# Kernel tuning notes

Hardware: AMD Instinct MI355X
Metric: run time of the kernel (lower is better)

The kernel has to match this reference:

```python
import jax, jax.numpy as jnp
import numpy as np

N_HEAD = 16
D_HEAD = 64
N_GROUPS = 4
D_EMBED = 1024
ROPE_N = 32
B, T = 2, 2048


def apply_rope(x, cos, sin):
    # x: (..., T, ROPE_N); cos/sin: (T, ROPE_N) broadcast over leading dims
    h = x.shape[-1]
    x1, x2 = x[..., : h // 2], x[..., h // 2 :]
    rotated = jnp.concatenate((-x2, x1), axis=-1)
    return (x * cos + rotated * sin).astype(x.dtype)


def setup_inputs() -> dict:
    key = jax.random.key(0)
    k1, k2, k3, k4, k5 = jax.random.split(key, 5)
    return {
        "x": jax.random.normal(k1, (B, T, D_EMBED), dtype=jnp.float32),
        "cos": jax.random.uniform(k2, (T, ROPE_N), dtype=jnp.float32),
        "sin": jax.random.uniform(k3, (T, ROPE_N), dtype=jnp.float32),
        "mask": jnp.ones((B, T), dtype=bool),  # unused by the original forward (passes None to SDPA)
        "Wqkv": jax.random.normal(k4, (D_EMBED, (N_HEAD + 2 * N_GROUPS) * D_HEAD), dtype=jnp.float32) * 0.02,
        "Wout": jax.random.normal(k5, (N_HEAD * D_HEAD, D_EMBED), dtype=jnp.float32) * 0.02,
    }


def reference(x, cos, sin, mask, Wqkv, Wout):
    Bv, Tv, _ = x.shape
    q_per_kv = N_HEAD // N_GROUPS  # 4
    total_qkv = q_per_kv + 2       # 6

    qkv = jnp.einsum("btc,cf->btf", x, Wqkv)  # (B, T, 1536)
    qkv = qkv.reshape(Bv, Tv, N_GROUPS, total_qkv, D_HEAD)
    qkv = jnp.transpose(qkv, (0, 2, 3, 1, 4))  # (B, G, total_qkv, T, d)

    q = qkv[:, :, :q_per_kv]           # (B, G, q_per_kv, T, d)
    k = qkv[:, :, q_per_kv : q_per_kv + 1]  # (B, G, 1, T, d)
    v = qkv[:, :, q_per_kv + 1 :]           # (B, G, 1, T, d)

    # GQA expand (1 < groups < heads)
    k = jnp.broadcast_to(k, (Bv, N_GROUPS, q_per_kv, Tv, D_HEAD))
    v = jnp.broadcast_to(v, (Bv, N_GROUPS, q_per_kv, Tv, D_HEAD))

    q = q.reshape(Bv, N_HEAD, Tv, D_HEAD)
    k = k.reshape(Bv, N_HEAD, Tv, D_HEAD)
    v = v.reshape(Bv, N_HEAD, Tv, D_HEAD)

    # partial RoPE on the first ROPE_N dims of each head
    q = jnp.concatenate((apply_rope(q[..., :ROPE_N], cos, sin), q[..., ROPE_N:]), axis=-1)
    k = jnp.concatenate((apply_rope(k[..., :ROPE_N], cos, sin), k[..., ROPE_N:]), axis=-1)

    scale = 1.0 / np.sqrt(D_HEAD).astype(np.float32)
    scores = jnp.einsum("bhtd,bhsd->bhts", q, k) * scale
    attn = jax.nn.softmax(scores, axis=-1)
    y = jnp.einsum("bhts,bhsd->bhtd", attn, v)   # (B, H, T, d)
    y = jnp.transpose(y, (0, 2, 1, 3)).reshape(Bv, Tv, N_HEAD * D_HEAD)
    return jnp.einsum("btf,fc->btc", y, Wout)
```

## Files before the change

### kernel.cpp

```cpp
#include <hip/hip_runtime.h>
#include <hip/hip_bf16.h>
#include <math.h>

#define BATCH   2
#define TSEQ    2048
#define DEMBED  1024
#define NHEAD   16
#define DHEAD   64
#define NGROUP  4
#define ROPEN   32
#define FQKV    1536
#define MROWS   (BATCH*TSEQ)

typedef __attribute__((ext_vector_type(8))) short short8;
typedef __attribute__((ext_vector_type(4))) float floatx4;

__device__ __forceinline__ void split_pack8(const float* f, uint4& h4, uint4& l4) {
    uint u[8], lu[8];
    #pragma unroll
    for (int j = 0; j < 8; ++j) {
        u[j] = __float_as_uint(f[j]);
        float lf = f[j] - __uint_as_float(u[j] & 0xffff0000u);
        lu[j] = __float_as_uint(lf);
    }
    h4.x = __builtin_amdgcn_perm(u[1], u[0], 0x07060302u);
    h4.y = __builtin_amdgcn_perm(u[3], u[2], 0x07060302u);
    h4.z = __builtin_amdgcn_perm(u[5], u[4], 0x07060302u);
    h4.w = __builtin_amdgcn_perm(u[7], u[6], 0x07060302u);
    l4.x = __builtin_amdgcn_perm(lu[1], lu[0], 0x07060302u);
    l4.y = __builtin_amdgcn_perm(lu[3], lu[2], 0x07060302u);
    l4.z = __builtin_amdgcn_perm(lu[5], lu[4], 0x07060302u);
    l4.w = __builtin_amdgcn_perm(lu[7], lu[6], 0x07060302u);
}

__device__ __forceinline__ void rtn_pack8(const float* f, uint4& h4) {
    uint t[8];
    #pragma unroll
    for (int j = 0; j < 8; ++j)
        t[j] = __float_as_uint(f[j]) + 0x8000u;
    h4.x = __builtin_amdgcn_perm(t[1], t[0], 0x07060302u);
    h4.y = __builtin_amdgcn_perm(t[3], t[2], 0x07060302u);
    h4.z = __builtin_amdgcn_perm(t[5], t[4], 0x07060302u);
    h4.w = __builtin_amdgcn_perm(t[7], t[6], 0x07060302u);
}

__device__ __forceinline__ uint pk_bf16x2(float f0, float f1) {
    uint u0 = __float_as_uint(f0) + 0x8000u;
    uint u1 = __float_as_uint(f1) + 0x8000u;
    return __builtin_amdgcn_perm(u1, u0, 0x07060302u);
}

__device__ __forceinline__ float fast_exp2(float x) {
    float r;
    asm("v_exp_f32 %0, %1" : "=v"(r) : "v"(x));
    return r;
}

__device__ __forceinline__ void lds_async16(void* lds, const void* gp) {
    __builtin_amdgcn_global_load_lds(
        (const __attribute__((address_space(1))) unsigned int*)gp,
        (__attribute__((address_space(3))) unsigned int*)lds,
        16, 0, 0);
}


__global__ __launch_bounds__(256) void conv_xy(const float* __restrict__ in,
                                               char* __restrict__ img) {
    const int tid = threadIdx.x;
    const int c   = blockIdx.x & 15;
    const int mt  = blockIdx.x >> 4;
    const int r    = tid >> 1;
    const int half = tid & 1;

    const float* src = in + (size_t)(mt*128 + r)*1024 + c*64 + half*32;
    float f[32];
    #pragma unroll
    for (int u = 0; u < 8; ++u)
        *(float4*)(f + 4*u) = *(const float4*)(src + 4*u);

    char* tile = img + ((size_t)(mt*16 + c)) * 32768;
    #pragma unroll
    for (int cc = 0; cc < 4; ++cc) {
        uint4 h4, l4;
        split_pack8(f + cc*8, h4, l4);
        int j    = half*4 + cc;
        int phys = j ^ (r & 7);
        *(uint4*)(tile + r*128 + phys*16)         = h4;
        *(uint4*)(tile + 16384 + r*128 + phys*16) = l4;
    }
}

__global__ __launch_bounds__(256) void conv_w(const float* __restrict__ W,
                                              int N,
                                              char* __restrict__ img) {
    __shared__ float Lf[64][132];
    const int tid = threadIdx.x;
    const int c   = blockIdx.x;
    const int nt  = blockIdx.y;

    {
        const int kk = tid >> 2;
        const int nc = (tid & 3) * 32;
        const float* src = W + (size_t)(c*64 + kk)*N + nt*128 + nc;
        #pragma unroll
        for (int u = 0; u < 8; ++u)
            *(float4*)(&Lf[kk][nc + 4*u]) = *(const float4*)(src + 4*u);
    }
    __syncthreads();

    char* tile = img + ((size_t)(nt*16 + c)) * 32768;
    #pragma unroll
    for (int rep = 0; rep < 4; ++rep) {
        int idx = rep*256 + tid;
        int n = idx & 127;
        int j = idx >> 7;
        float v[8];
        #pragma unroll
        for (int i = 0; i < 8; ++i) v[i] = Lf[j*8 + i][n];
        uint4 h4, l4;
        split_pack8(v, h4, l4);
        int phys = j ^ (n & 7);
        *(uint4*)(tile + n*128 + phys*16)         = h4;
        *(uint4*)(tile + 16384 + n*128 + phys*16) = l4;
    }
}

struct GemmAcc { floatx4 a[4][4]; };

__device__ __forceinline__ void gemm_mfma_core(const char* __restrict__ Aimg,
                                               const char* __restrict__ Bimg,
                                               char* smem, int mt, int nt,
                                               int tid, GemmAcc& G) {
    const int wv = tid >> 6;
    const int wm = wv & 1, wn = wv >> 1;
    const int lane = tid & 63;
    const int qd = lane >> 4, cl = lane & 15;
    const int wslot = (tid & 192) * 16;

    #pragma unroll
    for (int tm = 0; tm < 4; ++tm)
        #pragma unroll
        for (int tn = 0; tn < 4; ++tn)
            G.a[tm][tn] = (floatx4){0.f, 0.f, 0.f, 0.f};

    for (int c = 0; c < 16; ++c) {
        __syncthreads();
        {
            const uint4* gA = (const uint4*)(Aimg + ((size_t)(mt*16 + c)) * 32768) + tid;
            const uint4* gB = (const uint4*)(Bimg + ((size_t)(nt*16 + c)) * 32768) + tid;
            #pragma unroll
            for (int j = 0; j < 8; ++j) {
                lds_async16(smem + j*4096 + wslot,         gA + j*256);
                lds_async16(smem + 32768 + j*4096 + wslot, gB + j*256);
            }
        }
        __syncthreads();

        #pragma unroll
        for (int s = 0; s < 2; ++s) {
            const int phys = ((s*4 + qd) ^ (cl & 7)) * 16;
            short8 ah[4], al[4], bh[4], bl[4];
            #pragma unroll
            for (int tt = 0; tt < 4; ++tt) {
                const int rA = wm*64 + 16*tt + cl;
                ah[tt] = *(const short8*)(smem + rA*128 + phys);
                al[tt] = *(const short8*)(smem + 16384 + rA*128 + phys);
                const int rB = wn*64 + 16*tt + cl;
                bh[tt] = *(const short8*)(smem + 32768 + rB*128 + phys);
                bl[tt] = *(const short8*)(smem + 49152 + rB*128 + phys);
            }
            #pragma unroll
            for (int tm = 0; tm < 4; ++tm)
                #pragma unroll
                for (int tn = 0; tn < 4; ++tn) {
                    G.a[tm][tn] = __builtin_amdgcn_mfma_f32_16x16x32_bf16(ah[tm], bh[tn], G.a[tm][tn], 0, 0, 0);
                    G.a[tm][tn] = __builtin_amdgcn_mfma_f32_16x16x32_bf16(al[tm], bh[tn], G.a[tm][tn], 0, 0, 0);
                    G.a[tm][tn] = __builtin_amdgcn_mfma_f32_16x16x32_bf16(ah[tm], bl[tn], G.a[tm][tn], 0, 0, 0);
                }
        }
    }
}

__global__ __launch_bounds__(256, 2) void gemm_qkv_mfma(const char* __restrict__ Aimg,
                                                        const char* __restrict__ Bimg,
                                                        const float* __restrict__ cosp,
                                                        const float* __restrict__ sinp,
                                                        float* __restrict__ Qf,
                                                        ushort* __restrict__ Kimg,
                                                        ushort* __restrict__ Vimg) {
    __shared__ __align__(16) char smem[68608];
    const int tid = threadIdx.x;
    const int nt = blockIdx.x, mt = blockIdx.y;

    GemmAcc G;
    gemm_mfma_core(Aimg, Bimg, smem, mt, nt, tid, G);

    const int wv = tid >> 6;
    const int wm = wv & 1, wn = wv >> 1;
    const int lane = tid & 63;
    const int qd = lane >> 4, cl = lane & 15;

    const int slice = nt*2 + wn;
    const int g  = slice / 6;
    const int jj = slice % 6;
    const int b  = mt >> 4;

    if (jj != 5) {
        #pragma unroll
        for (int tm = 0; tm < 4; ++tm)
            #pragma unroll
            for (int r = 0; r < 4; ++r) {
                int m = mt*128 + wm*64 + 16*tm + 4*qd + r;
                int t = m & 2047;
                float c1 = cosp[t*ROPEN + cl],      s1 = sinp[t*ROPEN + cl];
                float c2 = cosp[t*ROPEN + 16 + cl], s2 = sinp[t*ROPEN + 16 + cl];
                float x1 = G.a[tm][0][r], x2 = G.a[tm][1][r];
                G.a[tm][0][r] = x1*c1 - x2*s1;
                G.a[tm][1][r] = x2*c2 + x1*s2;
            }
    }

    if (jj < 4) {
        #pragma unroll
        for (int tm = 0; tm < 4; ++tm)
            #pragma unroll
            for (int tn = 0; tn < 4; ++tn)
                #pragma unroll
                for (int r = 0; r < 4; ++r) {
                    int m = mt*128 + wm*64 + 16*tm + 4*qd + r;
                    Qf[(size_t)m*1024 + (g*4 + jj)*64 + 16*tn + cl] = G.a[tm][tn][r];
                }
    } else {
        float* Lw = (float*)(smem + wv*17152);
        __syncthreads();
        #pragma unroll
        for (int tm = 0; tm < 4; ++tm)
            #pragma unroll
            for (int tn = 0; tn < 4; ++tn)
                #pragma unroll
                for (int r = 0; r < 4; ++r)
                    Lw[(16*tm + 4*qd + r)*67 + 16*tn + cl] = G.a[tm][tn][r];
        __syncthreads();

        const int cloc = (mt & 15)*2 + wm;
        ushort* img = ((jj == 4) ? Kimg : Vimg)
                      + (size_t)(b*4 + g)*262144 + (size_t)cloc*8192;
        if (jj == 4) {
            const int rr = lane;
            float f[8];
            #pragma unroll
            for (int ch = 0; ch < 8; ++ch) {
                *(float4*)f       = *(const float4*)(&Lw[rr*67 + ch*8]);
                *(float4*)(f + 4) = *(const float4*)(&Lw[rr*67 + ch*8 + 4]);
                uint4 h4, l4;
                split_pack8(f, h4, l4);
                int phys = ch ^ (rr & 7);
                *(uint4*)(img + rr*64 + phys*8)        = h4;
                *(uint4*)(img + 4096 + rr*64 + phys*8) = l4;
            }
        } else {
            const int d = lane;
            float f[8];
            #pragma unroll
            for (int ch = 0; ch < 8; ++ch) {
                const int kb = 32*(ch >> 2) + 4*(ch & 3);
                #pragma unroll
                for (int i = 0; i < 4; ++i) f[i]     = Lw[(kb + i)*67 + d];
                #pragma unroll
                for (int i = 0; i < 4; ++i) f[4 + i] = Lw[(kb + 16 + i)*67 + d];
                uint4 h4;
                rtn_pack8(f, h4);
                int phys = ch ^ (d & 7);
                *(uint4*)(img + d*64 + phys*8) = h4;
            }
        }
    }
}

__global__ __launch_bounds__(256, 2) void gemm_out_mfma(const char* __restrict__ Aimg,
                                                        const char* __restrict__ Bimg,
                                                        float* __restrict__ C) {
    __shared__ __align__(16) char smem[49152];
    const int tid = threadIdx.x;
    const int nt = blockIdx.x, mt = blockIdx.y;

    const int wv = tid >> 6;
    const int wm = wv & 1, wn = wv >> 1;
    const int lane = tid & 63;
    const int qd = lane >> 4, cl = lane & 15;
    const int wslot = (tid & 192) * 16;

    floatx4 acc[2][4];
    #pragma unroll
    for (int tm = 0; tm < 2; ++tm)
        #pragma unroll
        for (int tn = 0; tn < 4; ++tn)
            acc[tm][tn] = (floatx4){0.f, 0.f, 0.f, 0.f};

    for (int c = 0; c < 16; ++c) {
        __syncthreads();
        {
            const char* sA = Aimg + ((size_t)((mt >> 1)*16 + c))*32768
                                  + (mt & 1)*8192 + (size_t)tid*16;
            const char* sB = Bimg + ((size_t)(nt*16 + c))*32768 + (size_t)tid*16;
            lds_async16(smem + wslot,          sA);
            lds_async16(smem + 4096  + wslot,  sA + 4096);
            lds_async16(smem + 8192  + wslot,  sA + 16384);
            lds_async16(smem + 12288 + wslot,  sA + 16384 + 4096);
            #pragma unroll
            for (int j = 0; j < 4; ++j) {
                lds_async16(smem + 16384 + j*4096 + wslot, sB + j*4096);
                lds_async16(smem + 32768 + j*4096 + wslot, sB + 16384 + j*4096);
            }
        }
        __syncthreads();

        #pragma unroll
        for (int s = 0; s < 2; ++s) {
            const int phys = ((s*4 + qd) ^ (cl & 7)) * 16;
            short8 ah[2], al[2], bh[4], bl[4];
            #pragma unroll
            for (int tt = 0; tt < 2; ++tt) {
                const int rA = wm*32 + 16*tt + cl;
                ah[tt] = *(const short8*)(smem + rA*128 + phys);
                al[tt] = *(const short8*)(smem + 8192 + rA*128 + phys);
            }
            #pragma unroll
            for (int tt = 0; tt < 4; ++tt) {
                const int rB = wn*64 + 16*tt + cl;
                bh[tt] = *(const short8*)(smem + 16384 + rB*128 + phys);
                bl[tt] = *(const short8*)(smem + 32768 + rB*128 + phys);
            }
            #pragma unroll
            for (int tm = 0; tm < 2; ++tm)
                #pragma unroll
                for (int tn = 0; tn < 4; ++tn) {
                    acc[tm][tn] = __builtin_amdgcn_mfma_f32_16x16x32_bf16(ah[tm], bh[tn], acc[tm][tn], 0, 0, 0);
                    acc[tm][tn] = __builtin_amdgcn_mfma_f32_16x16x32_bf16(al[tm], bh[tn], acc[tm][tn], 0, 0, 0);
                    acc[tm][tn] = __builtin_amdgcn_mfma_f32_16x16x32_bf16(ah[tm], bl[tn], acc[tm][tn], 0, 0, 0);
                }
        }
    }

    #pragma unroll
    for (int tm = 0; tm < 2; ++tm)
        #pragma unroll
        for (int tn = 0; tn < 4; ++tn)
            #pragma unroll
            for (int r = 0; r < 4; ++r) {
                int m = mt*64 + wm*32 + 16*tm + 4*qd + r;
                int n = nt*128 + wn*64 + 16*tn + cl;
                C[(size_t)m*1024 + n] = acc[tm][tn][r];
            }
}

__global__ __launch_bounds__(512, 4) void attn15(const float* __restrict__ Qf,
                                                 const char* __restrict__ Kimg,
                                                 const char* __restrict__ Vimg,
                                                 char* __restrict__ Yimg) {
    __shared__ __align__(16) char smem[49152];

    const int tid  = threadIdx.x;
    const int wv8  = tid >> 6;
    const int grp  = wv8 >> 2;
    const int wq   = wv8 & 3;
    const int lane = tid & 63;
    const int qd   = lane >> 4;
    const int cl   = lane & 15;

    const int bg    = blockIdx.x & 7;
    const int inner = blockIdx.x >> 3;
    const int hj    = inner >> 4;
    const int qt    = inner & 15;
    const int b = bg >> 2, g = bg & 3;
    const int h = g*4 + hj;

    short8 qh[2][2], ql[2][2];
    #pragma unroll
    for (int rb = 0; rb < 2; ++rb) {
        const float* qp = Qf + (size_t)(b*2048 + qt*128 + wq*32 + rb*16 + cl)*1024
                             + h*64 + 8*qd;
        #pragma unroll
        for (int s = 0; s < 2; ++s) {
            float f[8];
            *(float4*)f       = *(const float4*)(qp + 32*s);
            *(float4*)(f + 4) = *(const float4*)(qp + 32*s + 4);
            #pragma unroll
            for (int i = 0; i < 8; ++i) f[i] *= 0.125f * 1.44269504088896f;
            uint4 h4, l4;
            split_pack8(f, h4, l4);
            qh[rb][s] = __builtin_bit_cast(short8, h4);
            ql[rb][s] = __builtin_bit_cast(short8, l4);
        }
    }

    floatx4 accOT[2][4] = {};
    float lsum[2] = {};

    const char* Kg0 = Kimg + (size_t)bg*524288;
    const char* Vg0 = Vimg + (size_t)bg*524288;
    const int wslot = wv8 << 10;

    int voff[4];
    #pragma unroll
    for (int tt = 0; tt < 4; ++tt)
        voff[tt] = (16*tt + cl)*128 + (((4*grp + qd) ^ (cl & 7))*16);

    {
        const char* ksrc = Kg0 + (size_t)tid*16;
        lds_async16(smem + wslot,        ksrc);
        lds_async16(smem + 8192 + wslot, ksrc + 8192);
        lds_async16(smem + 32768 + wslot, Vg0 + (size_t)tid*16);
    }

    for (int c = 0; c < TSEQ/64; ++c) {
        __syncthreads();
        const int buf = c & 1;

        if (c + 1 < TSEQ/64) {
            const char* ksrc = Kg0 + (size_t)(c+1)*16384 + (size_t)tid*16;
            const char* vsrc = Vg0 + (size_t)(c+1)*16384 + (size_t)tid*16;
            lds_async16(smem + (1-buf)*16384 + wslot,        ksrc);
            lds_async16(smem + (1-buf)*16384 + 8192 + wslot, ksrc + 8192);
            lds_async16(smem + 32768 + (1-buf)*8192 + wslot, vsrc);
        }
        const char* Kl = smem + buf*16384;
        const char* Vl = smem + 32768 + buf*8192;

        floatx4 accST[2][2] = {};
        __builtin_amdgcn_s_setprio(1);
        #pragma unroll
        for (int s = 0; s < 2; ++s) {
            #pragma unroll
            for (int tt = 0; tt < 2; ++tt) {
                const int off = (32*grp + 16*tt + cl)*128
                              + (((4*s + qd) ^ (cl & 7))*16);
                short8 kh = *(const short8*)(Kl + off);
                short8 kl = *(const short8*)(Kl + 8192 + off);
                #pragma unroll
                for (int rb = 0; rb < 2; ++rb) {
                    accST[rb][tt] = __builtin_amdgcn_mfma_f32_16x16x32_bf16(kh, qh[rb][s], accST[rb][tt], 0, 0, 0);
                    accST[rb][tt] = __builtin_amdgcn_mfma_f32_16x16x32_bf16(kh, ql[rb][s], accST[rb][tt], 0, 0, 0);
                    accST[rb][tt] = __builtin_amdgcn_mfma_f32_16x16x32_bf16(kl, qh[rb][s], accST[rb][tt], 0, 0, 0);
                }
            }
        }
        __builtin_amdgcn_s_setprio(0);

        short8 pa[2];
        #pragma unroll
        for (int rb = 0; rb < 2; ++rb) {
            float p[8];
            #pragma unroll
            for (int tt = 0; tt < 2; ++tt)
                #pragma unroll
                for (int r = 0; r < 4; ++r)
                    p[4*tt + r] = fast_exp2(accST[rb][tt][r]);
            lsum[rb] += ((p[0] + p[1]) + (p[2] + p[3]))
                      + ((p[4] + p[5]) + (p[6] + p[7]));
            uint4 paw;
            paw.x = pk_bf16x2(p[0], p[1]);
            paw.y = pk_bf16x2(p[2], p[3]);
            paw.z = pk_bf16x2(p[4], p[5]);
            paw.w = pk_bf16x2(p[6], p[7]);
            pa[rb] = __builtin_bit_cast(short8, paw);
        }

        __builtin_amdgcn_s_setprio(1);
        #pragma unroll
        for (int tt = 0; tt < 4; ++tt) {
            short8 vh = *(const short8*)(Vl + voff[tt]);
            #pragma unroll
            for (int rb = 0; rb < 2; ++rb)
                accOT[rb][tt] = __builtin_amdgcn_mfma_f32_16x16x32_bf16(vh, pa[rb], accOT[rb][tt], 0, 0, 0);
        }
        __builtin_amdgcn_s_setprio(0);
    }

    __syncthreads();
    float* Pb = (float*)smem;
    if (grp == 1) {
        #pragma unroll
        for (int rb = 0; rb < 2; ++rb) {
            float* dst = Pb + (size_t)(((wq*2 + rb)*64) + lane)*17;
            #pragma unroll
            for (int tt = 0; tt < 4; ++tt)
                #pragma unroll
                for (int r = 0; r < 4; ++r)
                    dst[4*tt + r] = accOT[rb][tt][r];
            dst[16] = lsum[rb];
        }
    }
    __syncthreads();
    float inv[2] = {1.f, 1.f};
    if (grp == 0) {
        #pragma unroll
        for (int rb = 0; rb < 2; ++rb) {
            const float* sp = Pb + (size_t)(((wq*2 + rb)*64) + lane)*17;
            #pragma unroll
            for (int tt = 0; tt < 4; ++tt)
                #pragma unroll
                for (int r = 0; r < 4; ++r)
                    accOT[rb][tt][r] += sp[4*tt + r];
            float l = lsum[rb] + sp[16];
            l += __shfl_xor(l, 16);
            l += __shfl_xor(l, 32);
            inv[rb] = 1.0f / l;
        }
    }
    __syncthreads();
    float* Lt = (float*)smem;
    if (grp == 0) {
        #pragma unroll
        for (int rb = 0; rb < 2; ++rb) {
            const int row = wq*32 + rb*16 + cl;
            #pragma unroll
            for (int tt = 0; tt < 4; ++tt)
                #pragma unroll
                for (int r = 0; r < 4; ++r)
                    Lt[row*66 + 16*tt + 4*qd + r] = accOT[rb][tt][r] * inv[rb];
        }
    }
    __syncthreads();
    {
        char* tile = Yimg + (size_t)((b*16 + qt)*16 + h) * 32768;
        #pragma unroll
        for (int cc = 0; cc < 2; ++cc) {
            const int idx = tid*2 + cc;
            const int r0 = idx >> 3;
            const int j  = idx & 7;
            float f[8];
            #pragma unroll
            for (int u = 0; u < 4; ++u)
                *(float2*)(f + 2*u) = *(const float2*)(&Lt[r0*66 + j*8 + 2*u]);
            uint4 h4, l4;
            split_pack8(f, h4, l4);
            int phys = j ^ (r0 & 7);
            *(uint4*)(tile + r0*128 + phys*16)         = h4;
            *(uint4*)(tile + 16384 + r0*128 + phys*16) = l4;
        }
    }
}

extern "C" void kernel_launch(void* const* d_in, const int* in_sizes, int n_in,
                              void* d_out, int out_size, void* d_ws, size_t ws_size,
                              hipStream_t stream) {
    const float* x    = (const float*)d_in[0];
    const float* cosp = (const float*)d_in[1];
    const float* sinp = (const float*)d_in[2];
    const float* Wqkv = (const float*)d_in[4];
    const float* Wout = (const float*)d_in[5];
    float* out = (float*)d_out;

    char* ws = (char*)d_ws;
    float*  Qf    = (float*)(ws);
    ushort* Kimg  = (ushort*)(ws + ((size_t)16<<20));
    ushort* Vimg  = (ushort*)(ws + ((size_t)20<<20));
    char*   Bo    = ws + ((size_t)24<<20);
    char*   Ximg  = ws + ((size_t)28<<20);
    char*   Bq    = ws + ((size_t)44<<20);
    char*   Yimg  = ws + ((size_t)28<<20);

    conv_xy<<<512, 256, 0, stream>>>(x, Ximg);
    conv_w<<<dim3(16, 12), 256, 0, stream>>>(Wqkv, FQKV, Bq);
    conv_w<<<dim3(16, 8), 256, 0, stream>>>(Wout, DEMBED, Bo);
    gemm_qkv_mfma<<<dim3(12, 32), 256, 0, stream>>>(Ximg, Bq, cosp, sinp,
                                                    Qf, Kimg, Vimg);
    attn15<<<512, 512, 0, stream>>>(Qf, (const char*)Kimg, (const char*)Vimg,
                                    Yimg);
    gemm_out_mfma<<<dim3(8, 64), 256, 0, stream>>>(Yimg, Bo, out);
}
```

Before: 224.2 us.

## Double-buffer LDS tiles in both GEMM kernels with half-K chunks

Both MFMA GEMM kernels now split each K chunk into two half-chunks and double-buffer them in LDS. The async global-to-LDS copy of the next half-chunk is issued before computing on the current one, and one of the two barriers per iteration is dropped. Global reads use a new per-thread swizzled offset so LDS reads follow a 64-byte-row XOR pattern. The aim is to hide load latency behind MFMA work, at the cost of twice as many loop iterations and more address registers, and the pattern relies on the async copies having completed by the single barrier.

New measurement: 229.0 us. 1.02x slower.

```diff
diff --git a/kernel.cpp b/kernel.cpp
--- a/kernel.cpp
+++ b/kernel.cpp
@@ -136,6 +136,19 @@
     const int lane = tid & 63;
     const int qd = lane >> 4, cl = lane & 15;
     const int wslot = (tid & 192) * 16;
+    const int xorv  = (cl >> 1) & 3;
+
+    int soff[2][2];
+    #pragma unroll
+    for (int jj = 0; jj < 2; ++jj) {
+        const int ci   = jj*256 + tid;
+        const int row  = ci >> 2;
+        const int slot = ci & 3;
+        const int j    = slot ^ ((row >> 1) & 3);
+        #pragma unroll
+        for (int sp = 0; sp < 2; ++sp)
+            soff[sp][jj] = row*128 + (((j + 4*sp) ^ (row & 7)) * 16);
+    }
 
     #pragma unroll
     for (int tm = 0; tm < 4; ++tm)
@@ -143,41 +156,55 @@
         for (int tn = 0; tn < 4; ++tn)
             G.a[tm][tn] = (floatx4){0.f, 0.f, 0.f, 0.f};
 
-    for (int c = 0; c < 16; ++c) {
+    {
+        const char* gA = Aimg + (size_t)(mt*16) * 32768;
+        const char* gB = Bimg + (size_t)(nt*16) * 32768;
+        #pragma unroll
+        for (int jj = 0; jj < 2; ++jj) {
+            lds_async16(smem + jj*4096 + wslot,         gA + soff[0][jj]);
+            lds_async16(smem + 8192  + jj*4096 + wslot, gA + 16384 + soff[0][jj]);
+            lds_async16(smem + 16384 + jj*4096 + wslot, gB + soff[0][jj]);
+            lds_async16(smem + 24576 + jj*4096 + wslot, gB + 16384 + soff[0][jj]);
+        }
+    }
+
+    for (int c = 0; c < 32; ++c) {
         __syncthreads();
-        {
-            const uint4* gA = (const uint4*)(Aimg + ((size_t)(mt*16 + c)) * 32768) + tid;
-            const uint4* gB = (const uint4*)(Bimg + ((size_t)(nt*16 + c)) * 32768) + tid;
-            #pragma unroll
-            for (int j = 0; j < 8; ++j) {
-                lds_async16(smem + j*4096 + wslot,         gA + j*256);
-                lds_async16(smem + 32768 + j*4096 + wslot, gB + j*256);
-            }
-        }
-        __syncthreads();
-
-        #pragma unroll
-        for (int s = 0; s < 2; ++s) {
-            const int phys = ((s*4 + qd) ^ (cl & 7)) * 16;
-            short8 ah[4], al[4], bh[4], bl[4];
-            #pragma unroll
-            for (int tt = 0; tt < 4; ++tt) {
-                const int rA = wm*64 + 16*tt + cl;
-                ah[tt] = *(const short8*)(smem + rA*128 + phys);
-                al[tt] = *(const short8*)(smem + 16384 + rA*128 + phys);
-                const int rB = wn*64 + 16*tt + cl;
-                bh[tt] = *(const short8*)(smem + 32768 + rB*128 + phys);
-                bl[tt] = *(const short8*)(smem + 49152 + rB*128 + phys);
-            }
-            #pragma unroll
-            for (int tm = 0; tm < 4; ++tm)
-                #pragma unroll
-                for (int tn = 0; tn < 4; ++tn) {
-                    G.a[tm][tn] = __builtin_amdgcn_mfma_f32_16x16x32_bf16(ah[tm], bh[tn], G.a[tm][tn], 0, 0, 0);
-                    G.a[tm][tn] = __builtin_amdgcn_mfma_f32_16x16x32_bf16(al[tm], bh[tn], G.a[tm][tn], 0, 0, 0);
-                    G.a[tm][tn] = __builtin_amdgcn_mfma_f32_16x16x32_bf16(ah[tm], bl[tn], G.a[tm][tn], 0, 0, 0);
-                }
-        }
+        const int buf = c & 1;
+        if (c + 1 < 32) {
+            const int cn = c + 1;
+            const char* gA = Aimg + (size_t)(mt*16 + (cn >> 1)) * 32768;
+            const char* gB = Bimg + (size_t)(nt*16 + (cn >> 1)) * 32768;
+            char* dst = smem + (1 - buf)*32768;
+            const int sp = cn & 1;
+            #pragma unroll
+            for (int jj = 0; jj < 2; ++jj) {
+                lds_async16(dst + jj*4096 + wslot,         gA + soff[sp][jj]);
+                lds_async16(dst + 8192  + jj*4096 + wslot, gA + 16384 + soff[sp][jj]);
+                lds_async16(dst + 16384 + jj*4096 + wslot, gB + soff[sp][jj]);
+                lds_async16(dst + 24576 + jj*4096 + wslot, gB + 16384 + soff[sp][jj]);
+            }
+        }
+        const char* S = smem + buf*32768;
+
+        short8 ah[4], al[4], bh[4], bl[4];
+        #pragma unroll
+        for (int tt = 0; tt < 4; ++tt) {
+            const int ra = (wm*64 + 16*tt + cl)*64 + ((qd ^ xorv)*16);
+            ah[tt] = *(const short8*)(S + ra);
+            al[tt] = *(const short8*)(S + 8192 + ra);
+            const int rb = (wn*64 + 16*tt + cl)*64 + ((qd ^ xorv)*16);
+            bh[tt] = *(const short8*)(S + 16384 + rb);
+            bl[tt] = *(const short8*)(S + 24576 + rb);
+        }
+        #pragma unroll
+        for (int tm = 0; tm < 4; ++tm)
+            #pragma unroll
+            for (int tn = 0; tn < 4; ++tn) {
+                G.a[tm][tn] = __builtin_amdgcn_mfma_f32_16x16x32_bf16(ah[tm], bh[tn], G.a[tm][tn], 0, 0, 0);
+                G.a[tm][tn] = __builtin_amdgcn_mfma_f32_16x16x32_bf16(al[tm], bh[tn], G.a[tm][tn], 0, 0, 0);
+                G.a[tm][tn] = __builtin_amdgcn_mfma_f32_16x16x32_bf16(ah[tm], bl[tn], G.a[tm][tn], 0, 0, 0);
+            }
     }
 }
 
@@ -289,6 +316,26 @@
     const int lane = tid & 63;
     const int qd = lane >> 4, cl = lane & 15;
     const int wslot = (tid & 192) * 16;
+    const int xorv  = (cl >> 1) & 3;
+
+    int aoff[2];
+    {
+        const int row = tid >> 2, slot = tid & 3;
+        const int j = slot ^ ((row >> 1) & 3);
+        #pragma unroll
+        for (int sp = 0; sp < 2; ++sp)
+            aoff[sp] = row*128 + (((j + 4*sp) ^ (row & 7)) * 16);
+    }
+    int boff[2][2];
+    #pragma unroll
+    for (int jj = 0; jj < 2; ++jj) {
+        const int ci = jj*256 + tid;
+        const int row = ci >> 2, slot = ci & 3;
+        const int j = slot ^ ((row >> 1) & 3);
+        #pragma unroll
+        for (int sp = 0; sp < 2; ++sp)
+            boff[sp][jj] = row*128 + (((j + 4*sp) ^ (row & 7)) * 16);
+    }
 
     floatx4 acc[2][4];
     #pragma unroll
@@ -297,49 +344,59 @@
         for (int tn = 0; tn < 4; ++tn)
             acc[tm][tn] = (floatx4){0.f, 0.f, 0.f, 0.f};
 
-    for (int c = 0; c < 16; ++c) {
+    {
+        const char* gA = Aimg + (size_t)((mt >> 1)*16)*32768 + (mt & 1)*8192;
+        const char* gB = Bimg + (size_t)(nt*16)*32768;
+        lds_async16(smem + wslot,        gA + aoff[0]);
+        lds_async16(smem + 4096 + wslot, gA + 16384 + aoff[0]);
+        #pragma unroll
+        for (int jj = 0; jj < 2; ++jj) {
+            lds_async16(smem + 8192  + jj*4096 + wslot, gB + boff[0][jj]);
+            lds_async16(smem + 16384 + jj*4096 + wslot, gB + 16384 + boff[0][jj]);
+        }
+    }
+
+    for (int c = 0; c < 32; ++c) {
         __syncthreads();
-        {
-            const char* sA = Aimg + ((size_t)((mt >> 1)*16 + c))*32768
-                                  + (mt & 1)*8192 + (size_t)tid*16;
-            const char* sB = Bimg + ((size_t)(nt*16 + c))*32768 + (size_t)tid*16;
-            lds_async16(smem + wslot,          sA);
-            lds_async16(smem + 4096  + wslot,  sA + 4096);
-            lds_async16(smem + 8192  + wslot,  sA + 16384);
-            lds_async16(smem + 12288 + wslot,  sA + 16384 + 4096);
-            #pragma unroll
-            for (int j = 0; j < 4; ++j) {
-                lds_async16(smem + 16384 + j*4096 + wslot, sB + j*4096);
-                lds_async16(smem + 32768 + j*4096 + wslot, sB + 16384 + j*4096);
-            }
-        }
-        __syncthreads();
-
-        #pragma unroll
-        for (int s = 0; s < 2; ++s) {
-            const int phys = ((s*4 + qd) ^ (cl & 7)) * 16;
-            short8 ah[2], al[2], bh[4], bl[4];
-            #pragma unroll
-            for (int tt = 0; tt < 2; ++tt) {
-                const int rA = wm*32 + 16*tt + cl;
-                ah[tt] = *(const short8*)(smem + rA*128 + phys);
-                al[tt] = *(const short8*)(smem + 8192 + rA*128 + phys);
-            }
-            #pragma unroll
-            for (int tt = 0; tt < 4; ++tt) {
-                const int rB = wn*64 + 16*tt + cl;
-                bh[tt] = *(const short8*)(smem + 16384 + rB*128 + phys);
-                bl[tt] = *(const short8*)(smem + 32768 + rB*128 + phys);
-            }
-            #pragma unroll
-            for (int tm = 0; tm < 2; ++tm)
-                #pragma unroll
-                for (int tn = 0; tn < 4; ++tn) {
-                    acc[tm][tn] = __builtin_amdgcn_mfma_f32_16x16x32_bf16(ah[tm], bh[tn], acc[tm][tn], 0, 0, 0);
-                    acc[tm][tn] = __builtin_amdgcn_mfma_f32_16x16x32_bf16(al[tm], bh[tn], acc[tm][tn], 0, 0, 0);
-                    acc[tm][tn] = __builtin_amdgcn_mfma_f32_16x16x32_bf16(ah[tm], bl[tn], acc[tm][tn], 0, 0, 0);
-                }
-        }
+        const int buf = c & 1;
+        if (c + 1 < 32) {
+            const int cn = c + 1;
+            const char* gA = Aimg + (size_t)((mt >> 1)*16 + (cn >> 1))*32768
+                                  + (mt & 1)*8192;
+            const char* gB = Bimg + (size_t)(nt*16 + (cn >> 1))*32768;
+            char* dst = smem + (1 - buf)*24576;
+            const int sp = cn & 1;
+            lds_async16(dst + wslot,        gA + aoff[sp]);
+            lds_async16(dst + 4096 + wslot, gA + 16384 + aoff[sp]);
+            #pragma unroll
+            for (int jj = 0; jj < 2; ++jj) {
+                lds_async16(dst + 8192  + jj*4096 + wslot, gB + boff[sp][jj]);
+                lds_async16(dst + 16384 + jj*4096 + wslot, gB + 16384 + boff[sp][jj]);
+            }
+        }
+        const char* S = smem + buf*24576;
+
+        short8 ah[2], al[2], bh[4], bl[4];
+        #pragma unroll
+        for (int tt = 0; tt < 2; ++tt) {
+            const int ra = (wm*32 + 16*tt + cl)*64 + ((qd ^ xorv)*16);
+            ah[tt] = *(const short8*)(S + ra);
+            al[tt] = *(const short8*)(S + 4096 + ra);
+        }
+        #pragma unroll
+        for (int tt = 0; tt < 4; ++tt) {
+            const int rb = (wn*64 + 16*tt + cl)*64 + ((qd ^ xorv)*16);
+            bh[tt] = *(const short8*)(S + 8192 + rb);
+            bl[tt] = *(const short8*)(S + 16384 + rb);
+        }
+        #pragma unroll
+        for (int tm = 0; tm < 2; ++tm)
+            #pragma unroll
+            for (int tn = 0; tn < 4; ++tn) {
+                acc[tm][tn] = __builtin_amdgcn_mfma_f32_16x16x32_bf16(ah[tm], bh[tn], acc[tm][tn], 0, 0, 0);
+                acc[tm][tn] = __builtin_amdgcn_mfma_f32_16x16x32_bf16(al[tm], bh[tn], acc[tm][tn], 0, 0, 0);
+                acc[tm][tn] = __builtin_amdgcn_mfma_f32_16x16x32_bf16(ah[tm], bl[tn], acc[tm][tn], 0, 0, 0);
+            }
     }
 
     #pragma unroll
```
